# Performance work log

Hardware: AMD Instinct MI355X
Metric: run time of the kernel (lower is better)

Reference implementation:

```python
import jax, jax.numpy as jnp
import numpy as np

N_NODES = 40000
N_EDGES = 640000
IN_CH, HID_CH, OUT_CH = 128, 128, 64
NEG_SLOPE = 0.2  # PyG GATConv default


def _add_self_loops(src, dst, n):
    loop = jnp.arange(n, dtype=src.dtype)
    return jnp.concatenate([src, loop]), jnp.concatenate([dst, loop])


def gcn_conv(x, src, dst, W, b, n):
    # PyG GCNConv: add self-loops, symmetric degree norm, then aggregate.
    h = x @ W                                   # [N, F_out]
    s, d = _add_self_loops(src, dst, n)
    deg = jax.ops.segment_sum(jnp.ones_like(d, dtype=h.dtype), d, num_segments=n)
    dinv = jnp.where(deg > 0, jax.lax.rsqrt(deg), 0.0)
    norm = dinv[s] * dinv[d]                    # [E+N]
    msg = h[s] * norm[:, None]                  # gather + scale
    out = jax.ops.segment_sum(msg, d, num_segments=n)
    return out + b


def gat_conv(x, src, dst, W, a_src, a_dst, b, n):
    # PyG GATConv, heads=1: self-loops, edge-wise LeakyReLU attention logits,
    # softmax over incoming edges per dst node, weighted scatter-add.
    h = x @ W                                   # [N, F_out]
    s, d = _add_self_loops(src, dst, n)
    logit = jax.nn.leaky_relu((h @ a_src)[s] + (h @ a_dst)[d], NEG_SLOPE)  # [E+N]
    mx = jax.ops.segment_max(logit, d, num_segments=n)
    e = jnp.exp(logit - mx[d])
    z = jax.ops.segment_sum(e, d, num_segments=n)
    alpha = e / z[d]
    out = jax.ops.segment_sum(h[s] * alpha[:, None], d, num_segments=n)
    return out + b


def setup_inputs() -> dict:
    key = jax.random.key(0)
    ks = jax.random.split(key, 16)
    x = jax.random.normal(ks[0], (N_NODES, IN_CH), dtype=jnp.float32)
    edge_index = jax.random.randint(ks[1], (2, N_EDGES), 0, N_NODES, dtype=jnp.int64 if jax.config.jax_enable_x64 else jnp.int32)
    glorot = lambda k, fi, fo: jax.random.normal(k, (fi, fo), jnp.float32) * np.sqrt(2.0 / (fi + fo))
    params = {
        'W1': glorot(ks[2], IN_CH, HID_CH),   'b1': jnp.zeros((HID_CH,), jnp.float32),
        'Wg1': glorot(ks[3], HID_CH, HID_CH), 'ag1_src': jax.random.normal(ks[4], (HID_CH,), jnp.float32) * 0.1,
        'ag1_dst': jax.random.normal(ks[5], (HID_CH,), jnp.float32) * 0.1, 'bg1': jnp.zeros((HID_CH,), jnp.float32),
        'W2': glorot(ks[6], HID_CH, OUT_CH),  'b2': jnp.zeros((OUT_CH,), jnp.float32),
        'Wg2': glorot(ks[7], OUT_CH, OUT_CH), 'ag2_src': jax.random.normal(ks[8], (OUT_CH,), jnp.float32) * 0.1,
        'ag2_dst': jax.random.normal(ks[9], (OUT_CH,), jnp.float32) * 0.1, 'bg2': jnp.zeros((OUT_CH,), jnp.float32),
    }
    return {'x': x, 'edge_index': edge_index, **params}


def reference(x, edge_index, W1, b1, Wg1, ag1_src, ag1_dst, bg1, W2, b2, Wg2, ag2_src, ag2_dst, bg2):
    n = x.shape[0]
    src, dst = edge_index[0], edge_index[1]
    h = jax.nn.relu(gcn_conv(x, src, dst, W1, b1, n))
    # dropout(p=0.5) is identity in eval mode
    encoded = gat_conv(h, src, dst, Wg1, ag1_src, ag1_dst, bg1, n)
    h = jax.nn.relu(gcn_conv(encoded, src, dst, W2, b2, n))
    decoded = gat_conv(h, src, dst, Wg2, ag2_src, ag2_dst, bg2, n)
    return encoded, decoded
```

## Files before the change

### kernel.cpp

```cpp
#include <hip/hip_runtime.h>

#define NN 40000
#define NE 640000
#define NSB ((NN + 255) / 256)
#define NNP (NN + 64)

typedef unsigned int uint32;
typedef unsigned short ushort;
typedef __attribute__((ext_vector_type(8))) short bf16x8;
typedef __attribute__((ext_vector_type(4))) float f32x4;

static __device__ __forceinline__ float lrelu(float x) { return x > 0.0f ? x : 0.2f * x; }

static __device__ __forceinline__ float wave_max(float v) {
    for (int off = 32; off; off >>= 1) v = fmaxf(v, __shfl_xor(v, off));
    return v;
}
static __device__ __forceinline__ float wave_sum(float v) {
    for (int off = 32; off; off >>= 1) v += __shfl_xor(v, off);
    return v;
}

static __device__ __forceinline__ uint32 bfr(float x) {
    uint32 u = __float_as_uint(x);
    return u + 0x7FFFu + ((u >> 16) & 1u);
}
static __device__ __forceinline__ ushort bf16of(float x) { return (ushort)(bfr(x) >> 16); }
static __device__ __forceinline__ uint32 pack2(float a, float b) {
    return (bfr(a) >> 16) | (bfr(b) & 0xFFFF0000u);
}
static __device__ __forceinline__ float lo16(uint32 v) { return __uint_as_float(v << 16); }
static __device__ __forceinline__ float hi16(uint32 v) { return __uint_as_float(v & 0xFFFF0000u); }

__global__ void k_cast(const float* __restrict__ x, ushort* __restrict__ xb,
                       const float* __restrict__ W1, const float* __restrict__ Wg1,
                       const float* __restrict__ W2, const float* __restrict__ Wg2,
                       ushort* __restrict__ t1, ushort* __restrict__ tg1,
                       ushort* __restrict__ t2, ushort* __restrict__ tg2) {
    if (blockIdx.y == 0) {
        int base = (blockIdx.x * 256 + threadIdx.x) * 4;
        if (base < NN * 128) {
            float4 v = *(const float4*)&x[base];
            ushort4 o;
            o.x = bf16of(v.x);
            o.y = bf16of(v.y);
            o.z = bf16of(v.z);
            o.w = bf16of(v.w);
            *(ushort4*)&xb[base] = o;
        }
        return;
    }
    const float* W;
    ushort* T;
    int K, N;
    switch (blockIdx.y) {
        case 1: W = W1; T = t1; K = 128; N = 128; break;
        case 2: W = Wg1; T = tg1; K = 128; N = 128; break;
        case 3: W = W2; T = t2; K = 128; N = 64; break;
        default: W = Wg2; T = tg2; K = 64; N = 64; break;
    }
    int idx = blockIdx.x * 256 + threadIdx.x;
    if (idx < K * N) {
        int n = idx / K, k = idx % K;
        T[idx] = bf16of(W[k * N + n]);
    }
}

template <int FIN, int FOUT, bool GAT>
__global__ __launch_bounds__(256) void k_gemm_mfma(const ushort* __restrict__ Xb,
                                                   const ushort* __restrict__ Wt,
                                                   ushort* __restrict__ Y16,
                                                   const float* __restrict__ a_s,
                                                   const float* __restrict__ a_d,
                                                   float* __restrict__ asrc,
                                                   float* __restrict__ adst) {
    constexpr int NT = FOUT / 16;
    const int w = threadIdx.x >> 6, lane = threadIdx.x & 63;
    const int row0 = blockIdx.x * 128 + w * 32;
    const int lr = lane & 15;
    const int lk = (lane >> 4) * 8;

    f32x4 acc[2][NT];
#pragma unroll
    for (int mt = 0; mt < 2; ++mt)
#pragma unroll
        for (int nt = 0; nt < NT; ++nt) acc[mt][nt] = (f32x4){0.f, 0.f, 0.f, 0.f};

#pragma unroll
    for (int ks = 0; ks < FIN / 32; ++ks) {
        bf16x8 a[2], b[NT];
#pragma unroll
        for (int mt = 0; mt < 2; ++mt)
            a[mt] = *(const bf16x8*)&Xb[(size_t)(row0 + mt * 16 + lr) * FIN + ks * 32 + lk];
#pragma unroll
        for (int nt = 0; nt < NT; ++nt)
            b[nt] = *(const bf16x8*)&Wt[(size_t)(nt * 16 + lr) * FIN + ks * 32 + lk];
#pragma unroll
        for (int mt = 0; mt < 2; ++mt)
#pragma unroll
            for (int nt = 0; nt < NT; ++nt)
                acc[mt][nt] =
                    __builtin_amdgcn_mfma_f32_16x16x32_bf16(a[mt], b[nt], acc[mt][nt], 0, 0, 0);
    }

    const int rbase = (lane >> 4) * 4;
#pragma unroll
    for (int mt = 0; mt < 2; ++mt)
#pragma unroll
        for (int nt = 0; nt < NT; ++nt) {
            int col = nt * 16 + lr;
#pragma unroll
            for (int i = 0; i < 4; ++i) {
                int r = row0 + mt * 16 + rbase + i;
                if (r < NN) Y16[(size_t)r * FOUT + col] = bf16of(acc[mt][nt][i]);
            }
        }

    if (GAT) {
#pragma unroll
        for (int mt = 0; mt < 2; ++mt)
#pragma unroll
            for (int i = 0; i < 4; ++i) {
                float ss = 0.0f, dd = 0.0f;
#pragma unroll
                for (int nt = 0; nt < NT; ++nt) {
                    float v = acc[mt][nt][i];
                    ss = fmaf(v, a_s[nt * 16 + lr], ss);
                    dd = fmaf(v, a_d[nt * 16 + lr], dd);
                }
#pragma unroll
                for (int off = 1; off < 16; off <<= 1) {
                    ss += __shfl_xor(ss, off);
                    dd += __shfl_xor(dd, off);
                }
                if (lr == 0) {
                    int r = row0 + mt * 16 + rbase + i;
                    if (r < NN) {
                        asrc[r] = ss;
                        adst[r] = dd;
                    }
                }
            }
    }
}

__global__ void k_zero_int(int* __restrict__ p, int n) {
    int i = blockIdx.x * blockDim.x + threadIdx.x;
    if (i < n) p[i] = 0;
}
__global__ void k_count(const int* __restrict__ dst, int* __restrict__ cnt) {
    int e = blockIdx.x * blockDim.x + threadIdx.x;
    if (e < NE) atomicAdd(&cnt[dst[e]], 1);
}
__global__ void k_bsum(const int* __restrict__ cnt, int* __restrict__ bsum) {
    __shared__ int wsums[4];
    int i = blockIdx.x * 256 + threadIdx.x;
    int v = (i < NN) ? cnt[i] : 0;
    for (int off = 32; off; off >>= 1) v += __shfl_down(v, off);
    if ((threadIdx.x & 63) == 0) wsums[threadIdx.x >> 6] = v;
    __syncthreads();
    if (threadIdx.x == 0) bsum[blockIdx.x] = wsums[0] + wsums[1] + wsums[2] + wsums[3];
}
__global__ void k_scanpart(const int* __restrict__ bsum, int* __restrict__ bofs,
                           int* __restrict__ rowptr) {
    __shared__ int s[256];
    int t = threadIdx.x;
    int v = (t < NSB) ? bsum[t] : 0;
    s[t] = v;
    __syncthreads();
    for (int off = 1; off < 256; off <<= 1) {
        int u = (t >= off) ? s[t - off] : 0;
        __syncthreads();
        s[t] += u;
        __syncthreads();
    }
    if (t < NSB) bofs[t] = s[t] - v;
    if (t == 0) rowptr[NN] = NE;
}
__global__ void k_scatter(const int* __restrict__ cnt, const int* __restrict__ bofs,
                          int* __restrict__ rowptr, int* __restrict__ cursor,
                          float* __restrict__ dinv) {
    __shared__ int wsums[4];
    int t = threadIdx.x;
    int lane = t & 63, w = t >> 6;
    int i = blockIdx.x * 256 + t;
    int v = (i < NN) ? cnt[i] : 0;
    int x = v;
    for (int off = 1; off < 64; off <<= 1) {
        int u = __shfl_up(x, off);
        if (lane >= off) x += u;
    }
    if (lane == 63) wsums[w] = x;
    __syncthreads();
    int wofs = 0;
    for (int k = 0; k < w; ++k) wofs += wsums[k];
    int excl = bofs[blockIdx.x] + wofs + x - v;
    if (i < NN) {
        rowptr[i] = excl;
        cursor[i] = excl;
        dinv[i] = rsqrtf(1.0f + (float)v);
    }
}
__global__ void k_fill(const int* __restrict__ src, const int* __restrict__ dst,
                       int* __restrict__ cursor, int* __restrict__ csr_src) {
    int e = blockIdx.x * blockDim.x + threadIdx.x;
    if (e < NE) {
        int p = atomicAdd(&cursor[dst[e]], 1);
        csr_src[p] = src[e];
    }
}

static __device__ __forceinline__ void gath128(const uint32* __restrict__ h16, int lane, int myi,
                                               float myw, int cnt, float* acc) {
    for (int j = 0; j < cnt; j += 8) {
        int s[8];
        float w[8];
#pragma unroll
        for (int u = 0; u < 8; ++u) {
            s[u] = __shfl(myi, j + u);
            w[u] = __shfl(myw, j + u);
        }
        uint32 v[8];
#pragma unroll
        for (int u = 0; u < 8; ++u) v[u] = h16[(size_t)s[u] * 64 + lane];
#pragma unroll
        for (int u = 0; u < 8; ++u) {
            acc[0] = fmaf(w[u], lo16(v[u]), acc[0]);
            acc[1] = fmaf(w[u], hi16(v[u]), acc[1]);
        }
    }
}
static __device__ __forceinline__ void gath64(const uint32* __restrict__ h16, int lane, int myi,
                                              float myw, int cnt, float* acc) {
    int hh = lane >> 5, cl = lane & 31;
    for (int j = 0; j < cnt; j += 16) {
        int s[8];
        float w[8];
#pragma unroll
        for (int u = 0; u < 8; ++u) {
            int e = j + 2 * u + hh;
            s[u] = __shfl(myi, e);
            w[u] = __shfl(myw, e);
        }
        uint32 v[8];
#pragma unroll
        for (int u = 0; u < 8; ++u) v[u] = h16[(size_t)s[u] * 32 + cl];
#pragma unroll
        for (int u = 0; u < 8; ++u) {
            acc[0] = fmaf(w[u], lo16(v[u]), acc[0]);
            acc[1] = fmaf(w[u], hi16(v[u]), acc[1]);
        }
    }
}

template <int F>
__global__ __launch_bounds__(256) void k_gcn_gather_w(const int* __restrict__ rowptr,
                                                      const int* __restrict__ csr_src,
                                                      const uint32* __restrict__ h16,
                                                      const float* __restrict__ dinv,
                                                      const float* __restrict__ b,
                                                      uint32* __restrict__ out16) {
    int node = blockIdx.x * 4 + (threadIdx.x >> 6);
    int lane = threadIdx.x & 63;
    int beg = rowptr[node], end = rowptr[node + 1];
    float dd = dinv[node];
    float acc[2] = {0.0f, 0.0f};

    for (int g = beg; g < end; g += 64) {
        int cnt = end - g;
        if (cnt > 64) cnt = 64;
        int myi = node;
        float myw = 0.0f;
        if (lane < cnt) {
            int s = __builtin_nontemporal_load(&csr_src[g + lane]);
            myi = s;
            myw = dinv[s];
        }
        if (F == 128)
            gath128(h16, lane, myi, myw, cnt, acc);
        else
            gath64(h16, lane, myi, myw, cnt, acc);
    }
    if (F == 128) {
        uint32 sv = h16[(size_t)node * 64 + lane];
        acc[0] = fmaf(dd, lo16(sv), acc[0]);
        acc[1] = fmaf(dd, hi16(sv), acc[1]);
        int c = lane * 2;
        float rx = fmaxf(fmaf(acc[0], dd, b[c]), 0.0f);
        float ry = fmaxf(fmaf(acc[1], dd, b[c + 1]), 0.0f);
        out16[(size_t)node * 64 + lane] = pack2(rx, ry);
    } else {
        acc[0] += __shfl_xor(acc[0], 32);
        acc[1] += __shfl_xor(acc[1], 32);
        if (lane < 32) {
            uint32 sv = h16[(size_t)node * 32 + lane];
            acc[0] = fmaf(dd, lo16(sv), acc[0]);
            acc[1] = fmaf(dd, hi16(sv), acc[1]);
            int c = lane * 2;
            float rx = fmaxf(fmaf(acc[0], dd, b[c]), 0.0f);
            float ry = fmaxf(fmaf(acc[1], dd, b[c + 1]), 0.0f);
            out16[(size_t)node * 32 + lane] = pack2(rx, ry);
        }
    }
}

template <int F, bool WB16>
__global__ __launch_bounds__(256) void k_gat_gather_w(const int* __restrict__ rowptr,
                                                      const int* __restrict__ csr_src,
                                                      const uint32* __restrict__ h16,
                                                      const float* __restrict__ asrc,
                                                      const float* __restrict__ adst,
                                                      const float* __restrict__ b,
                                                      float* __restrict__ out,
                                                      uint32* __restrict__ out16) {
    int node = blockIdx.x * 4 + (threadIdx.x >> 6);
    int lane = threadIdx.x & 63;
    int beg = rowptr[node], end = rowptr[node + 1];
    int deg = end - beg;
    float ad = adst[node];
    float slog = lrelu(asrc[node] + ad);
    float acc[2] = {0.0f, 0.0f};
    float wself;

    if (deg <= 64) {
        int myi = node;
        float logit = -1e30f;
        if (lane < deg) {
            myi = __builtin_nontemporal_load(&csr_src[beg + lane]);
            logit = lrelu(asrc[myi] + ad);
        }
        float m = fmaxf(slog, wave_max(logit));
        float e = (lane < deg) ? __expf(logit - m) : 0.0f;
        float z = wave_sum(e) + __expf(slog - m);
        float zi = 1.0f / z;
        float myw = e * zi;
        wself = __expf(slog - m) * zi;
        if (F == 128)
            gath128(h16, lane, myi, myw, deg, acc);
        else
            gath64(h16, lane, myi, myw, deg, acc);
    } else {
        float lm = slog;
        for (int j = beg + lane; j < end; j += 64) lm = fmaxf(lm, lrelu(asrc[csr_src[j]] + ad));
        float m = wave_max(lm);
        float lz = 0.0f;
        for (int j = beg + lane; j < end; j += 64)
            lz += __expf(lrelu(asrc[csr_src[j]] + ad) - m);
        float z = wave_sum(lz) + __expf(slog - m);
        float zi = 1.0f / z;
        wself = __expf(slog - m) * zi;
        for (int g = beg; g < end; g += 64) {
            int cnt = end - g;
            if (cnt > 64) cnt = 64;
            int myi = node;
            float myw = 0.0f;
            if (lane < cnt) {
                int s = csr_src[g + lane];
                myi = s;
                myw = __expf(lrelu(asrc[s] + ad) - m) * zi;
            }
            if (F == 128)
                gath128(h16, lane, myi, myw, cnt, acc);
            else
                gath64(h16, lane, myi, myw, cnt, acc);
        }
    }
    if (F == 128) {
        uint32 sv = h16[(size_t)node * 64 + lane];
        acc[0] = fmaf(wself, lo16(sv), acc[0]);
        acc[1] = fmaf(wself, hi16(sv), acc[1]);
        int c = lane * 2;
        float2 r;
        r.x = acc[0] + b[c];
        r.y = acc[1] + b[c + 1];
        *(float2*)&out[(size_t)node * 128 + c] = r;
        if (WB16) out16[(size_t)node * 64 + lane] = pack2(r.x, r.y);
    } else {
        acc[0] += __shfl_xor(acc[0], 32);
        acc[1] += __shfl_xor(acc[1], 32);
        if (lane < 32) {
            uint32 sv = h16[(size_t)node * 32 + lane];
            acc[0] = fmaf(wself, lo16(sv), acc[0]);
            acc[1] = fmaf(wself, hi16(sv), acc[1]);
            int c = lane * 2;
            float2 r;
            r.x = acc[0] + b[c];
            r.y = acc[1] + b[c + 1];
            *(float2*)&out[(size_t)node * 64 + c] = r;
            if (WB16) out16[(size_t)node * 32 + lane] = pack2(r.x, r.y);
        }
    }
}

extern "C" void kernel_launch(void* const* d_in, const int* in_sizes, int n_in,
                              void* d_out, int out_size, void* d_ws, size_t ws_size,
                              hipStream_t stream) {
    const float* x = (const float*)d_in[0];
    const int* src = (const int*)d_in[1];
    const int* dst = src + NE;
    const float* W1 = (const float*)d_in[2];
    const float* b1 = (const float*)d_in[3];
    const float* Wg1 = (const float*)d_in[4];
    const float* ag1s = (const float*)d_in[5];
    const float* ag1d = (const float*)d_in[6];
    const float* bg1 = (const float*)d_in[7];
    const float* W2 = (const float*)d_in[8];
    const float* b2 = (const float*)d_in[9];
    const float* Wg2 = (const float*)d_in[10];
    const float* ag2s = (const float*)d_in[11];
    const float* ag2d = (const float*)d_in[12];
    const float* bg2 = (const float*)d_in[13];

    float* enc = (float*)d_out;
    float* dec = enc + (size_t)NN * 128;

    ushort* m0 = (ushort*)d_ws;
    ushort* m1 = m0 + (size_t)NNP * 128;
    ushort* m2 = m1 + (size_t)NNP * 128;
    ushort* wt1 = m2 + (size_t)NNP * 128;
    ushort* wtg1 = wt1 + 128 * 128;
    ushort* wt2 = wtg1 + 128 * 128;
    ushort* wtg2 = wt2 + 64 * 128;
    float* dinv = (float*)(wtg2 + 64 * 64);
    float* asrc = dinv + NN;
    float* adst = asrc + NN;
    int* cnt = (int*)(adst + NN);
    int* rowptr = cnt + NN;
    int* cursor = rowptr + NN + 1;
    int* csr_src = cursor + NN;
    int* bsum = csr_src + NE;
    int* bofs = bsum + NSB;

    const int TB = 256;
    int gN = (NN + TB - 1) / TB;
    int gE = (NE + TB - 1) / TB;
    int gWave = NN / 4;
    int gM = (NN + 127) / 128;

    k_cast<<<dim3((NN * 128 / 4 + TB - 1) / TB, 5), TB, 0, stream>>>(x, m0, W1, Wg1, W2, Wg2,
                                                                     wt1, wtg1, wt2, wtg2);

    k_zero_int<<<gN, TB, 0, stream>>>(cnt, NN);
    k_count<<<gE, TB, 0, stream>>>(dst, cnt);
    k_bsum<<<NSB, 256, 0, stream>>>(cnt, bsum);
    k_scanpart<<<1, 256, 0, stream>>>(bsum, bofs, rowptr);
    k_scatter<<<NSB, 256, 0, stream>>>(cnt, bofs, rowptr, cursor, dinv);
    k_fill<<<gE, TB, 0, stream>>>(src, dst, cursor, csr_src);

    k_gemm_mfma<128, 128, false><<<gM, 256, 0, stream>>>(m0, wt1, m2, nullptr, nullptr, nullptr,
                                                         nullptr);
    k_gcn_gather_w<128><<<gWave, 256, 0, stream>>>(rowptr, csr_src, (uint32*)m2, dinv, b1,
                                                   (uint32*)m1);

    k_gemm_mfma<128, 128, true><<<gM, 256, 0, stream>>>(m1, wtg1, m2, ag1s, ag1d, asrc, adst);
    k_gat_gather_w<128, true><<<gWave, 256, 0, stream>>>(rowptr, csr_src, (uint32*)m2, asrc,
                                                         adst, bg1, enc, (uint32*)m0);

    k_gemm_mfma<128, 64, false><<<gM, 256, 0, stream>>>(m0, wt2, m2, nullptr, nullptr, nullptr,
                                                        nullptr);
    k_gcn_gather_w<64><<<gWave, 256, 0, stream>>>(rowptr, csr_src, (uint32*)m2, dinv, b2,
                                                  (uint32*)m1);

    k_gemm_mfma<64, 64, true><<<gM, 256, 0, stream>>>(m1, wtg2, m2, ag2s, ag2d, asrc, adst);
    k_gat_gather_w<64, false><<<gWave, 256, 0, stream>>>(rowptr, csr_src, (uint32*)m2, asrc,
                                                         adst, bg2, dec, (uint32*)m0);
}
```

Baseline: 235.2 us.

## Fuse CSR-building preprocessing kernels into one cooperative kernel with grid syncs

Replaces the six preprocessing launches (cast, zero, count, block-sum, scan, scatter, fill) with one cooperative kernel of 1024 blocks that uses grid-wide syncs between phases. The aim is to remove launch overhead and inter-kernel gaps for these small phases. In exchange it adds five grid barriers, which are costly, and uses a fixed grid with grid-stride loops, so less parallelism per phase.

Measured after the change: 782.9 us. +232.8%, slower.

```diff
diff --git a/kernel.cpp b/kernel.cpp
--- a/kernel.cpp
+++ b/kernel.cpp
@@ -1,9 +1,13 @@
 #include <hip/hip_runtime.h>
+#include <hip/hip_cooperative_groups.h>
+
+namespace cg = cooperative_groups;
 
 #define NN 40000
 #define NE 640000
 #define NSB ((NN + 255) / 256)
 #define NNP (NN + 64)
+#define PREB 1024
 
 typedef unsigned int uint32;
 typedef unsigned short ushort;
@@ -32,37 +36,117 @@
 static __device__ __forceinline__ float lo16(uint32 v) { return __uint_as_float(v << 16); }
 static __device__ __forceinline__ float hi16(uint32 v) { return __uint_as_float(v & 0xFFFF0000u); }
 
-__global__ void k_cast(const float* __restrict__ x, ushort* __restrict__ xb,
-                       const float* __restrict__ W1, const float* __restrict__ Wg1,
-                       const float* __restrict__ W2, const float* __restrict__ Wg2,
-                       ushort* __restrict__ t1, ushort* __restrict__ tg1,
-                       ushort* __restrict__ t2, ushort* __restrict__ tg2) {
-    if (blockIdx.y == 0) {
-        int base = (blockIdx.x * 256 + threadIdx.x) * 4;
-        if (base < NN * 128) {
-            float4 v = *(const float4*)&x[base];
-            ushort4 o;
-            o.x = bf16of(v.x);
-            o.y = bf16of(v.y);
-            o.z = bf16of(v.z);
-            o.w = bf16of(v.w);
-            *(ushort4*)&xb[base] = o;
-        }
-        return;
-    }
-    const float* W;
-    ushort* T;
-    int K, N;
-    switch (blockIdx.y) {
-        case 1: W = W1; T = t1; K = 128; N = 128; break;
-        case 2: W = Wg1; T = tg1; K = 128; N = 128; break;
-        case 3: W = W2; T = t2; K = 128; N = 64; break;
-        default: W = Wg2; T = tg2; K = 64; N = 64; break;
-    }
-    int idx = blockIdx.x * 256 + threadIdx.x;
-    if (idx < K * N) {
+struct PreArgs {
+    const float* x;
+    const float* W1;
+    const float* Wg1;
+    const float* W2;
+    const float* Wg2;
+    const int* src;
+    const int* dst;
+    ushort* xb;
+    ushort* t1;
+    ushort* tg1;
+    ushort* t2;
+    ushort* tg2;
+    int* cnt;
+    int* bsum;
+    int* bofs;
+    int* rowptr;
+    int* cursor;
+    float* dinv;
+    int* csr_src;
+};
+
+__global__ __launch_bounds__(256, 4) void k_pre(PreArgs a) {
+    cg::grid_group grid = cg::this_grid();
+    __shared__ int sh[256];
+    __shared__ int wsums[4];
+    const int T = PREB * 256;
+    const int tid = blockIdx.x * 256 + threadIdx.x;
+    const int t = threadIdx.x;
+
+    for (int i = tid; i < NN; i += T) a.cnt[i] = 0;
+    for (int q = tid; q < NN * 128 / 4; q += T) {
+        float4 v = *(const float4*)&a.x[q * 4];
+        ushort4 o;
+        o.x = bf16of(v.x);
+        o.y = bf16of(v.y);
+        o.z = bf16of(v.z);
+        o.w = bf16of(v.w);
+        *(ushort4*)&a.xb[q * 4] = o;
+    }
+    for (int i = tid; i < 45056; i += T) {
+        const float* W;
+        ushort* Tt;
+        int K, N, idx;
+        if (i < 16384) {
+            W = a.W1; Tt = a.t1; K = 128; N = 128; idx = i;
+        } else if (i < 32768) {
+            W = a.Wg1; Tt = a.tg1; K = 128; N = 128; idx = i - 16384;
+        } else if (i < 40960) {
+            W = a.W2; Tt = a.t2; K = 128; N = 64; idx = i - 32768;
+        } else {
+            W = a.Wg2; Tt = a.tg2; K = 64; N = 64; idx = i - 40960;
+        }
         int n = idx / K, k = idx % K;
-        T[idx] = bf16of(W[k * N + n]);
+        Tt[idx] = bf16of(W[k * N + n]);
+    }
+    grid.sync();
+
+    for (int e = tid; e < NE; e += T) atomicAdd(&a.cnt[a.dst[e]], 1);
+    grid.sync();
+
+    if (blockIdx.x < NSB) {
+        int i = blockIdx.x * 256 + t;
+        int v = (i < NN) ? a.cnt[i] : 0;
+        for (int off = 32; off; off >>= 1) v += __shfl_down(v, off);
+        if ((t & 63) == 0) wsums[t >> 6] = v;
+        __syncthreads();
+        if (t == 0) a.bsum[blockIdx.x] = wsums[0] + wsums[1] + wsums[2] + wsums[3];
+    }
+    grid.sync();
+
+    if (blockIdx.x == 0) {
+        int v = (t < NSB) ? a.bsum[t] : 0;
+        sh[t] = v;
+        __syncthreads();
+        for (int off = 1; off < 256; off <<= 1) {
+            int u = (t >= off) ? sh[t - off] : 0;
+            __syncthreads();
+            sh[t] += u;
+            __syncthreads();
+        }
+        if (t < NSB) a.bofs[t] = sh[t] - v;
+        if (t == 0) a.rowptr[NN] = NE;
+    }
+    grid.sync();
+
+    if (blockIdx.x < NSB) {
+        int lane = t & 63, w = t >> 6;
+        int i = blockIdx.x * 256 + t;
+        int v = (i < NN) ? a.cnt[i] : 0;
+        int x = v;
+        for (int off = 1; off < 64; off <<= 1) {
+            int u = __shfl_up(x, off);
+            if (lane >= off) x += u;
+        }
+        if (lane == 63) wsums[w] = x;
+        __syncthreads();
+        int wofs = 0;
+        for (int k = 0; k < w; ++k) wofs += wsums[k];
+        int excl = a.bofs[blockIdx.x] + wofs + x - v;
+        if (i < NN) {
+            a.rowptr[i] = excl;
+            a.cursor[i] = excl;
+            a.dinv[i] = rsqrtf(1.0f + (float)v);
+        }
+    }
+    grid.sync();
+
+    for (int e = tid; e < NE; e += T) {
+        int p = atomicAdd(&a.cursor[a.dst[e]], 1);
+        a.csr_src[p] = a.src[e];
     }
 }
 
@@ -141,72 +225,6 @@
                     }
                 }
             }
-    }
-}
-
-__global__ void k_zero_int(int* __restrict__ p, int n) {
-    int i = blockIdx.x * blockDim.x + threadIdx.x;
-    if (i < n) p[i] = 0;
-}
-__global__ void k_count(const int* __restrict__ dst, int* __restrict__ cnt) {
-    int e = blockIdx.x * blockDim.x + threadIdx.x;
-    if (e < NE) atomicAdd(&cnt[dst[e]], 1);
-}
-__global__ void k_bsum(const int* __restrict__ cnt, int* __restrict__ bsum) {
-    __shared__ int wsums[4];
-    int i = blockIdx.x * 256 + threadIdx.x;
-    int v = (i < NN) ? cnt[i] : 0;
-    for (int off = 32; off; off >>= 1) v += __shfl_down(v, off);
-    if ((threadIdx.x & 63) == 0) wsums[threadIdx.x >> 6] = v;
-    __syncthreads();
-    if (threadIdx.x == 0) bsum[blockIdx.x] = wsums[0] + wsums[1] + wsums[2] + wsums[3];
-}
-__global__ void k_scanpart(const int* __restrict__ bsum, int* __restrict__ bofs,
-                           int* __restrict__ rowptr) {
-    __shared__ int s[256];
-    int t = threadIdx.x;
-    int v = (t < NSB) ? bsum[t] : 0;
-    s[t] = v;
-    __syncthreads();
-    for (int off = 1; off < 256; off <<= 1) {
-        int u = (t >= off) ? s[t - off] : 0;
-        __syncthreads();
-        s[t] += u;
-        __syncthreads();
-    }
-    if (t < NSB) bofs[t] = s[t] - v;
-    if (t == 0) rowptr[NN] = NE;
-}
-__global__ void k_scatter(const int* __restrict__ cnt, const int* __restrict__ bofs,
-                          int* __restrict__ rowptr, int* __restrict__ cursor,
-                          float* __restrict__ dinv) {
-    __shared__ int wsums[4];
-    int t = threadIdx.x;
-    int lane = t & 63, w = t >> 6;
-    int i = blockIdx.x * 256 + t;
-    int v = (i < NN) ? cnt[i] : 0;
-    int x = v;
-    for (int off = 1; off < 64; off <<= 1) {
-        int u = __shfl_up(x, off);
-        if (lane >= off) x += u;
-    }
-    if (lane == 63) wsums[w] = x;
-    __syncthreads();
-    int wofs = 0;
-    for (int k = 0; k < w; ++k) wofs += wsums[k];
-    int excl = bofs[blockIdx.x] + wofs + x - v;
-    if (i < NN) {
-        rowptr[i] = excl;
-        cursor[i] = excl;
-        dinv[i] = rsqrtf(1.0f + (float)v);
-    }
-}
-__global__ void k_fill(const int* __restrict__ src, const int* __restrict__ dst,
-                       int* __restrict__ cursor, int* __restrict__ csr_src) {
-    int e = blockIdx.x * blockDim.x + threadIdx.x;
-    if (e < NE) {
-        int p = atomicAdd(&cursor[dst[e]], 1);
-        csr_src[p] = src[e];
     }
 }
 
@@ -431,21 +449,31 @@
     int* bsum = csr_src + NE;
     int* bofs = bsum + NSB;
 
-    const int TB = 256;
-    int gN = (NN + TB - 1) / TB;
-    int gE = (NE + TB - 1) / TB;
     int gWave = NN / 4;
     int gM = (NN + 127) / 128;
 
-    k_cast<<<dim3((NN * 128 / 4 + TB - 1) / TB, 5), TB, 0, stream>>>(x, m0, W1, Wg1, W2, Wg2,
-                                                                     wt1, wtg1, wt2, wtg2);
-
-    k_zero_int<<<gN, TB, 0, stream>>>(cnt, NN);
-    k_count<<<gE, TB, 0, stream>>>(dst, cnt);
-    k_bsum<<<NSB, 256, 0, stream>>>(cnt, bsum);
-    k_scanpart<<<1, 256, 0, stream>>>(bsum, bofs, rowptr);
-    k_scatter<<<NSB, 256, 0, stream>>>(cnt, bofs, rowptr, cursor, dinv);
-    k_fill<<<gE, TB, 0, stream>>>(src, dst, cursor, csr_src);
+    PreArgs pa;
+    pa.x = x;
+    pa.W1 = W1;
+    pa.Wg1 = Wg1;
+    pa.W2 = W2;
+    pa.Wg2 = Wg2;
+    pa.src = src;
+    pa.dst = dst;
+    pa.xb = m0;
+    pa.t1 = wt1;
+    pa.tg1 = wtg1;
+    pa.t2 = wt2;
+    pa.tg2 = wtg2;
+    pa.cnt = cnt;
+    pa.bsum = bsum;
+    pa.bofs = bofs;
+    pa.rowptr = rowptr;
+    pa.cursor = cursor;
+    pa.dinv = dinv;
+    pa.csr_src = csr_src;
+    void* kargs[] = {&pa};
+    hipLaunchCooperativeKernel((const void*)k_pre, dim3(PREB), dim3(256), kargs, 0, stream);
 
     k_gemm_mfma<128, 128, false><<<gM, 256, 0, stream>>>(m0, wt1, m2, nullptr, nullptr, nullptr,
                                                          nullptr);
```

## Replace ordered CSR scan with atomic segment allocation and per-edge ranks

Applied to the files above, without the earlier changes.

The CSR build drops the three-kernel prefix scan (bsum, scanpart, scatter) and the atomic cursor pass. k_count now records each edge's rank within its destination, one k_alloc kernel reserves each block's segment through a global atomic counter, and k_fill writes edges to base plus rank without atomics. The zeroing of the counters is folded into k_cast, and the gather kernels read an int2 (begin, end) per node instead of rowptr. This removes three launches and one atomic pass at the cost of a rank array in the workspace and segments placed in nondeterministic block order.

Measured after the change: 211.8 us (median of 2 runs). 1.11x faster.

```diff
diff --git a/kernel.cpp b/kernel.cpp
--- a/kernel.cpp
+++ b/kernel.cpp
@@ -36,7 +36,8 @@
                        const float* __restrict__ W1, const float* __restrict__ Wg1,
                        const float* __restrict__ W2, const float* __restrict__ Wg2,
                        ushort* __restrict__ t1, ushort* __restrict__ tg1,
-                       ushort* __restrict__ t2, ushort* __restrict__ tg2) {
+                       ushort* __restrict__ t2, ushort* __restrict__ tg2,
+                       int* __restrict__ cnt, int* __restrict__ gctr) {
     if (blockIdx.y == 0) {
         int base = (blockIdx.x * 256 + threadIdx.x) * 4;
         if (base < NN * 128) {
@@ -50,6 +51,12 @@
         }
         return;
     }
+    if (blockIdx.y == 5) {
+        int i = blockIdx.x * 256 + threadIdx.x;
+        if (i < NN) cnt[i] = 0;
+        if (i == 0) *gctr = 0;
+        return;
+    }
     const float* W;
     ushort* T;
     int K, N;
@@ -63,6 +70,45 @@
     if (idx < K * N) {
         int n = idx / K, k = idx % K;
         T[idx] = bf16of(W[k * N + n]);
+    }
+}
+
+__global__ void k_count(const int* __restrict__ dst, int* __restrict__ cnt,
+                        int* __restrict__ rank) {
+    int e = blockIdx.x * blockDim.x + threadIdx.x;
+    if (e < NE) rank[e] = atomicAdd(&cnt[dst[e]], 1);
+}
+__global__ void k_alloc(const int* __restrict__ cnt, int* __restrict__ gctr,
+                        int2* __restrict__ rseg, float* __restrict__ dinv) {
+    __shared__ int wsums[4];
+    __shared__ int sbase;
+    int t = threadIdx.x, lane = t & 63, w = t >> 6;
+    int i = blockIdx.x * 256 + t;
+    int v = (i < NN) ? cnt[i] : 0;
+    int x = v;
+    for (int off = 1; off < 64; off <<= 1) {
+        int u = __shfl_up(x, off);
+        if (lane >= off) x += u;
+    }
+    if (lane == 63) wsums[w] = x;
+    __syncthreads();
+    if (t == 0) sbase = atomicAdd(gctr, wsums[0] + wsums[1] + wsums[2] + wsums[3]);
+    __syncthreads();
+    int wofs = 0;
+    for (int k = 0; k < w; ++k) wofs += wsums[k];
+    int excl = sbase + wofs + x - v;
+    if (i < NN) {
+        rseg[i] = make_int2(excl, excl + v);
+        dinv[i] = rsqrtf(1.0f + (float)v);
+    }
+}
+__global__ void k_fill(const int* __restrict__ src, const int* __restrict__ dst,
+                       const int* __restrict__ rank, const int2* __restrict__ rseg,
+                       int* __restrict__ csr_src) {
+    int e = blockIdx.x * blockDim.x + threadIdx.x;
+    if (e < NE) {
+        int d = dst[e];
+        csr_src[rseg[d].x + rank[e]] = src[e];
     }
 }
 
@@ -144,72 +190,6 @@
     }
 }
 
-__global__ void k_zero_int(int* __restrict__ p, int n) {
-    int i = blockIdx.x * blockDim.x + threadIdx.x;
-    if (i < n) p[i] = 0;
-}
-__global__ void k_count(const int* __restrict__ dst, int* __restrict__ cnt) {
-    int e = blockIdx.x * blockDim.x + threadIdx.x;
-    if (e < NE) atomicAdd(&cnt[dst[e]], 1);
-}
-__global__ void k_bsum(const int* __restrict__ cnt, int* __restrict__ bsum) {
-    __shared__ int wsums[4];
-    int i = blockIdx.x * 256 + threadIdx.x;
-    int v = (i < NN) ? cnt[i] : 0;
-    for (int off = 32; off; off >>= 1) v += __shfl_down(v, off);
-    if ((threadIdx.x & 63) == 0) wsums[threadIdx.x >> 6] = v;
-    __syncthreads();
-    if (threadIdx.x == 0) bsum[blockIdx.x] = wsums[0] + wsums[1] + wsums[2] + wsums[3];
-}
-__global__ void k_scanpart(const int* __restrict__ bsum, int* __restrict__ bofs,
-                           int* __restrict__ rowptr) {
-    __shared__ int s[256];
-    int t = threadIdx.x;
-    int v = (t < NSB) ? bsum[t] : 0;
-    s[t] = v;
-    __syncthreads();
-    for (int off = 1; off < 256; off <<= 1) {
-        int u = (t >= off) ? s[t - off] : 0;
-        __syncthreads();
-        s[t] += u;
-        __syncthreads();
-    }
-    if (t < NSB) bofs[t] = s[t] - v;
-    if (t == 0) rowptr[NN] = NE;
-}
-__global__ void k_scatter(const int* __restrict__ cnt, const int* __restrict__ bofs,
-                          int* __restrict__ rowptr, int* __restrict__ cursor,
-                          float* __restrict__ dinv) {
-    __shared__ int wsums[4];
-    int t = threadIdx.x;
-    int lane = t & 63, w = t >> 6;
-    int i = blockIdx.x * 256 + t;
-    int v = (i < NN) ? cnt[i] : 0;
-    int x = v;
-    for (int off = 1; off < 64; off <<= 1) {
-        int u = __shfl_up(x, off);
-        if (lane >= off) x += u;
-    }
-    if (lane == 63) wsums[w] = x;
-    __syncthreads();
-    int wofs = 0;
-    for (int k = 0; k < w; ++k) wofs += wsums[k];
-    int excl = bofs[blockIdx.x] + wofs + x - v;
-    if (i < NN) {
-        rowptr[i] = excl;
-        cursor[i] = excl;
-        dinv[i] = rsqrtf(1.0f + (float)v);
-    }
-}
-__global__ void k_fill(const int* __restrict__ src, const int* __restrict__ dst,
-                       int* __restrict__ cursor, int* __restrict__ csr_src) {
-    int e = blockIdx.x * blockDim.x + threadIdx.x;
-    if (e < NE) {
-        int p = atomicAdd(&cursor[dst[e]], 1);
-        csr_src[p] = src[e];
-    }
-}
-
 static __device__ __forceinline__ void gath128(const uint32* __restrict__ h16, int lane, int myi,
                                                float myw, int cnt, float* acc) {
     for (int j = 0; j < cnt; j += 8) {
@@ -254,7 +234,7 @@
 }
 
 template <int F>
-__global__ __launch_bounds__(256) void k_gcn_gather_w(const int* __restrict__ rowptr,
+__global__ __launch_bounds__(256) void k_gcn_gather_w(const int2* __restrict__ rseg,
                                                       const int* __restrict__ csr_src,
                                                       const uint32* __restrict__ h16,
                                                       const float* __restrict__ dinv,
@@ -262,7 +242,8 @@
                                                       uint32* __restrict__ out16) {
     int node = blockIdx.x * 4 + (threadIdx.x >> 6);
     int lane = threadIdx.x & 63;
-    int beg = rowptr[node], end = rowptr[node + 1];
+    int2 se = rseg[node];
+    int beg = se.x, end = se.y;
     float dd = dinv[node];
     float acc[2] = {0.0f, 0.0f};
 
@@ -305,7 +286,7 @@
 }
 
 template <int F, bool WB16>
-__global__ __launch_bounds__(256) void k_gat_gather_w(const int* __restrict__ rowptr,
+__global__ __launch_bounds__(256) void k_gat_gather_w(const int2* __restrict__ rseg,
                                                       const int* __restrict__ csr_src,
                                                       const uint32* __restrict__ h16,
                                                       const float* __restrict__ asrc,
@@ -315,7 +296,8 @@
                                                       uint32* __restrict__ out16) {
     int node = blockIdx.x * 4 + (threadIdx.x >> 6);
     int lane = threadIdx.x & 63;
-    int beg = rowptr[node], end = rowptr[node + 1];
+    int2 se = rseg[node];
+    int beg = se.x, end = se.y;
     int deg = end - beg;
     float ad = adst[node];
     float slog = lrelu(asrc[node] + ad);
@@ -425,43 +407,38 @@
     float* asrc = dinv + NN;
     float* adst = asrc + NN;
     int* cnt = (int*)(adst + NN);
-    int* rowptr = cnt + NN;
-    int* cursor = rowptr + NN + 1;
-    int* csr_src = cursor + NN;
-    int* bsum = csr_src + NE;
-    int* bofs = bsum + NSB;
+    int* gctr = cnt + NN;
+    int2* rseg = (int2*)(gctr + 1);
+    int* rank = (int*)(rseg + NN);
+    int* csr_src = rank + NE;
 
     const int TB = 256;
-    int gN = (NN + TB - 1) / TB;
     int gE = (NE + TB - 1) / TB;
     int gWave = NN / 4;
     int gM = (NN + 127) / 128;
 
-    k_cast<<<dim3((NN * 128 / 4 + TB - 1) / TB, 5), TB, 0, stream>>>(x, m0, W1, Wg1, W2, Wg2,
-                                                                     wt1, wtg1, wt2, wtg2);
-
-    k_zero_int<<<gN, TB, 0, stream>>>(cnt, NN);
-    k_count<<<gE, TB, 0, stream>>>(dst, cnt);
-    k_bsum<<<NSB, 256, 0, stream>>>(cnt, bsum);
-    k_scanpart<<<1, 256, 0, stream>>>(bsum, bofs, rowptr);
-    k_scatter<<<NSB, 256, 0, stream>>>(cnt, bofs, rowptr, cursor, dinv);
-    k_fill<<<gE, TB, 0, stream>>>(src, dst, cursor, csr_src);
+    k_cast<<<dim3((NN * 128 / 4 + TB - 1) / TB, 6), TB, 0, stream>>>(
+        x, m0, W1, Wg1, W2, Wg2, wt1, wtg1, wt2, wtg2, cnt, gctr);
+
+    k_count<<<gE, TB, 0, stream>>>(dst, cnt, rank);
+    k_alloc<<<NSB, 256, 0, stream>>>(cnt, gctr, rseg, dinv);
+    k_fill<<<gE, TB, 0, stream>>>(src, dst, rank, rseg, csr_src);
 
     k_gemm_mfma<128, 128, false><<<gM, 256, 0, stream>>>(m0, wt1, m2, nullptr, nullptr, nullptr,
                                                          nullptr);
-    k_gcn_gather_w<128><<<gWave, 256, 0, stream>>>(rowptr, csr_src, (uint32*)m2, dinv, b1,
+    k_gcn_gather_w<128><<<gWave, 256, 0, stream>>>(rseg, csr_src, (uint32*)m2, dinv, b1,
                                                    (uint32*)m1);
 
     k_gemm_mfma<128, 128, true><<<gM, 256, 0, stream>>>(m1, wtg1, m2, ag1s, ag1d, asrc, adst);
-    k_gat_gather_w<128, true><<<gWave, 256, 0, stream>>>(rowptr, csr_src, (uint32*)m2, asrc,
-                                                         adst, bg1, enc, (uint32*)m0);
+    k_gat_gather_w<128, true><<<gWave, 256, 0, stream>>>(rseg, csr_src, (uint32*)m2, asrc, adst,
+                                                         bg1, enc, (uint32*)m0);
 
     k_gemm_mfma<128, 64, false><<<gM, 256, 0, stream>>>(m0, wt2, m2, nullptr, nullptr, nullptr,
                                                         nullptr);
-    k_gcn_gather_w<64><<<gWave, 256, 0, stream>>>(rowptr, csr_src, (uint32*)m2, dinv, b2,
+    k_gcn_gather_w<64><<<gWave, 256, 0, stream>>>(rseg, csr_src, (uint32*)m2, dinv, b2,
                                                   (uint32*)m1);
 
     k_gemm_mfma<64, 64, true><<<gM, 256, 0, stream>>>(m1, wtg2, m2, ag2s, ag2d, asrc, adst);
-    k_gat_gather_w<64, false><<<gWave, 256, 0, stream>>>(rowptr, csr_src, (uint32*)m2, asrc,
-                                                         adst, bg2, dec, (uint32*)m0);
-}
+    k_gat_gather_w<64, false><<<gWave, 256, 0, stream>>>(rseg, csr_src, (uint32*)m2, asrc, adst,
+                                                         bg2, dec, (uint32*)m0);
+}
```
